# Kernel tuning notes

Hardware: AMD Instinct MI355X
Metric: run time of the kernel (lower is better)

The kernel has to match this reference:

```python
import jax, jax.numpy as jnp
import numpy as np

MD = 4                  # corr_md
D = 2 * MD + 1          # patch_size = 9


def setup_inputs() -> dict:
    key = jax.random.key(0)
    k1, k2 = jax.random.split(key)
    b, c, h, w = 4, 128, 128, 256
    t1 = jax.random.normal(k1, (b, c, h, w), dtype=jnp.float32)
    t2 = jax.random.normal(k2, (b, c, h, w), dtype=jnp.float32)
    return {"t1": t1, "t2": t2}


def reference(t1, t2):
    # Local cost volume: for each displacement (di, dj) in [-MD, MD]^2,
    # out[b, p, y, x] = sum_c t1[b, c, y, x] * t2[b, c, y+di, x+dj]
    # with zero padding outside t2 (SpatialCorrelationSampler semantics,
    # kernel_size=1, stride=1, dilation_patch=1; no channel normalization).
    b, c, h, w = t1.shape
    t2p = jnp.pad(t2, ((0, 0), (0, 0), (MD, MD), (MD, MD)))
    # Loop over the fixed 9x9 displacement grid (81 small reductions);
    outs = [
        jnp.einsum('bchw,bchw->bhw', t1, t2p[:, :, i:i + h, j:j + w])
        for i in range(D) for j in range(D)
    ]
    return jnp.stack(outs, axis=1)  # [b, 81, h, w]
```

## Files before the change

### kernel.cpp

```cpp
#include <hip/hip_runtime.h>

#define NP 81
#define CC 128
#define HH 128
#define WW 256
#define YPAD 136
#define XPAD 272
#define WS_NEED (4ull * YPAD * XPAD * CC * 2ull)

#define SX 16
#define NBLK 1024

typedef __attribute__((ext_vector_type(4))) short bf16x4;
typedef __attribute__((ext_vector_type(8))) short short8;
typedef __attribute__((ext_vector_type(4))) float f32x4;
typedef __attribute__((ext_vector_type(16))) float f32x16;

__device__ __forceinline__ short f2bf(float f) {
    unsigned int u = __builtin_bit_cast(unsigned int, f);
    u += 0x7fffu + ((u >> 16) & 1u);
    return (short)(u >> 16);
}

__global__ __launch_bounds__(256) void prepass_t2t(const float* __restrict__ t2,
                                                   short* __restrict__ ws) {
    const int blk = blockIdx.x;
    const int hf  = blk & 1;
    const int row = blk >> 1;
    const int yp  = row % YPAD;
    const int b   = row / YPAD;
    const int tid = threadIdx.x;
    short* wrow = ws + (size_t)row * XPAD * CC;
    const int y2 = yp - 4;
    const short8 z = {0,0,0,0,0,0,0,0};
    if (y2 < 0 || y2 >= HH) {
        for (int u = tid + hf * 2176; u < 2176 + hf * 2176; u += 256)
            *(short8*)&wrow[(size_t)u * 8] = z;
        return;
    }
    if (tid < 128) {
        const int idx = hf * 8 + (tid >> 4);
        const int xp  = (idx < 4) ? idx : idx + 256;
        *(short8*)&wrow[(size_t)xp * CC + (tid & 15) * 8] = z;
    }
    const size_t plane = (size_t)HH * WW;
#pragma unroll
    for (int i = 0; i < 2; ++i) {
        const int u   = tid + i * 256;
        const int oct = hf * 8 + (u & 7);
        const int xq  = u >> 3;
        const float* p = t2 + ((size_t)(b * CC + oct * 8) * HH + y2) * WW + xq * 4;
        f32x4 v[8];
#pragma unroll
        for (int j = 0; j < 8; ++j) v[j] = *(const f32x4*)&p[(size_t)j * plane];
#pragma unroll
        for (int jj = 0; jj < 4; ++jj) {
            short8 s;
#pragma unroll
            for (int j = 0; j < 8; ++j) s[j] = f2bf(v[j][jj]);
            *(short8*)&wrow[(size_t)(4 + xq * 4 + jj) * CC + oct * 8] = s;
        }
    }
}

__global__ __launch_bounds__(1024) void corr_main16(
        const float* __restrict__ t1, const short* __restrict__ ws,
        float* __restrict__ out) {
    const int bid = blockIdx.x;
    const int sw  = (bid & 7) * (NBLK / 8) + (bid >> 3);
    const int xt = sw & 15;
    const int ys = (sw >> 4) & 15;
    const int b  = sw >> 8;
    const int X0 = xt * SX;
    const int y0 = ys * 8;

    const int tid  = threadIdx.x;
    const int lane = tid & 63;
    const int w    = tid >> 6;
    const int n    = lane & 31;
    const int g    = lane >> 5;

    __shared__ short sA[8 * SX * 128];
    __shared__ __align__(16) float obufs[16 * 9 * 20];

    const short* bp = ws + ((size_t)(b * YPAD + y0 + w) * XPAD + X0 + n) * CC
                    + g * 8;
    short8 bre[8];
#pragma unroll
    for (int kc = 0; kc < 8; ++kc)
        bre[kc] = *(const short8*)&bp[kc * 16];

    if (tid < 512) {
        const int oct = tid & 15;
        const int xq  = (tid >> 4) & 3;
        const int yy  = tid >> 6;
        const size_t plane = (size_t)HH * WW;
        const float* p = t1 + ((size_t)(b * CC + oct * 8) * HH + y0 + yy) * WW
                       + X0 + xq * 4;
#pragma unroll
        for (int h = 0; h < 2; ++h) {
            f32x4 v[4];
#pragma unroll
            for (int j = 0; j < 4; ++j)
                v[j] = *(const f32x4*)&p[(size_t)(h * 4 + j) * plane];
#pragma unroll
            for (int jj = 0; jj < 4; ++jj) {
                const int x = xq * 4 + jj;
                bf16x4 s;
#pragma unroll
                for (int j = 0; j < 4; ++j) s[j] = f2bf(v[j][jj]);
                *(bf16x4*)&sA[yy * 2048 + x * 128 + ((oct ^ x) * 8) + h * 4] = s;
            }
        }
    }
    __syncthreads();

    const int ylo = (w > 8) ? (w - 8) : 0;
    const int yhi = (w < 7) ? w : 7;
    float* ob = &obufs[w * 180];

    for (int yy = ylo; yy <= yhi; ++yy) {
        const int sbase = yy * 2048 + n * 128;

        f32x16 a;
#pragma unroll
        for (int q = 0; q < 16; ++q) a[q] = 0.f;
#pragma unroll
        for (int kc = 0; kc < 8; ++kc) {
            const short8 af = *(const short8*)
                &sA[sbase + (((kc * 2 + g) ^ (n & 15)) * 8)];
            a = __builtin_amdgcn_mfma_f32_32x32x16_bf16(af, bre[kc], a, 0, 0, 0);
        }

#pragma unroll
        for (int q = 0; q < 16; ++q) {
            const int m  = (q & 3) + 8 * (q >> 2) + 4 * g;
            const int dj = n - m;
            if (dj >= 0 && dj <= 8 && m < SX) ob[dj * 20 + m] = a[q];
        }

        const int di = w - yy;
        const int y  = y0 + yy;
        if (lane < 36) {
            const int dj = lane >> 2, xq = lane & 3;
            f32x4 vv = *(const f32x4*)&ob[dj * 20 + xq * 4];
            *(f32x4*)&out[((size_t)(b * NP + di * 9 + dj) * HH + y) * WW
                          + X0 + xq * 4] = vv;
        }
    }
}

#define FB_SX 24
#define FB_NXT 11
#define FB_NBLK (FB_NXT * 16 * 4)
__global__ __launch_bounds__(1024) void corr_fallback(
        const float* __restrict__ t1, const float* __restrict__ t2,
        float* __restrict__ out) {
    const int bid = blockIdx.x;
    const int sw  = (bid & 7) * (FB_NBLK / 8) + (bid >> 3);
    const int ys = sw & 15;
    const int v  = sw >> 4;
    const int xt = v % FB_NXT;
    const int b  = v / FB_NXT;
    const int X0 = xt * FB_SX;
    const int y0 = ys * 8;
    const int tid  = threadIdx.x;
    const int lane = tid & 63;
    const int w    = tid >> 6;
    const int n    = lane & 31;
    const int g    = lane >> 5;
    __shared__ short sA[8 * FB_SX * 128];
    __shared__ __align__(16) float obufs[16 * 9 * 28];
    const size_t plane = (size_t)HH * WW;
    const int r = y0 - 4 + w;
#pragma unroll
    for (int i = 0; i < 3; ++i) {
        const int unit = tid + i * 1024;
        const int x    = unit % FB_SX;
        const int rest = unit / FB_SX;
        const int oct  = rest & 15;
        const int yy   = rest >> 4;
        short8 pk = {0,0,0,0,0,0,0,0};
        if (X0 + x < WW) {
            const float* p = t1 + ((size_t)(b * CC + oct * 8) * HH + (y0 + yy)) * WW
                           + X0 + x;
#pragma unroll
            for (int j = 0; j < 8; ++j) pk[j] = f2bf(p[(size_t)j * plane]);
        }
        *(short8*)&sA[yy * (FB_SX * 128) + x * 128 + ((oct ^ (x & 15)) * 8)] = pk;
    }
    __syncthreads();
    const int x2 = X0 - 4 + n;
    const bool ok = (r >= 0) && (r < HH) && (x2 >= 0) && (x2 < WW);
    const int rc  = r  < 0 ? 0 : (r  > HH - 1 ? HH - 1 : r);
    const int xc  = x2 < 0 ? 0 : (x2 > WW - 1 ? WW - 1 : x2);
    const float* bp = t2 + ((size_t)(b * CC + g * 8) * HH + rc) * WW + xc;
    short8 bre[8];
#pragma unroll
    for (int kc = 0; kc < 8; ++kc) {
        short8 f;
#pragma unroll
        for (int j = 0; j < 8; ++j) f[j] = f2bf(bp[(size_t)(kc * 16 + j) * plane]);
        if (!ok) f = (short8){0,0,0,0,0,0,0,0};
        bre[kc] = f;
    }
    const int ylo = (w > 8) ? (w - 8) : 0;
    const int yhi = (w < 7) ? w : 7;
    float* ob = &obufs[w * 252];
    for (int yy = ylo; yy <= yhi; ++yy) {
        const int sbase = yy * (FB_SX * 128) + n * 128;
        f32x16 a;
#pragma unroll
        for (int q = 0; q < 16; ++q) a[q] = 0.f;
#pragma unroll
        for (int kc = 0; kc < 8; ++kc) {
            const short8 af = *(const short8*)
                &sA[sbase + (((kc * 2 + g) ^ (n & 15)) * 8)];
            a = __builtin_amdgcn_mfma_f32_32x32x16_bf16(af, bre[kc], a, 0, 0, 0);
        }
#pragma unroll
        for (int q = 0; q < 16; ++q) {
            const int m  = (q & 3) + 8 * (q >> 2) + 4 * g;
            const int dj = n - m;
            if (dj >= 0 && dj <= 8 && m < FB_SX) ob[dj * 28 + m] = a[q];
        }
        const int di = w - yy;
        const int y  = y0 + yy;
        if (lane < 54) {
            const int dj = lane / 6, xq = lane % 6;
            if (X0 + xq * 4 < WW) {
                f32x4 vv = *(const f32x4*)&ob[dj * 28 + xq * 4];
                *(f32x4*)&out[((size_t)(b * NP + di * 9 + dj) * HH + y) * WW
                              + X0 + xq * 4] = vv;
            }
        }
    }
}

extern "C" void kernel_launch(void* const* d_in, const int* in_sizes, int n_in,
                              void* d_out, int out_size, void* d_ws, size_t ws_size,
                              hipStream_t stream) {
    const float* t1 = (const float*)d_in[0];
    const float* t2 = (const float*)d_in[1];
    if (ws_size >= WS_NEED) {
        short* ws = (short*)d_ws;
        prepass_t2t<<<4 * YPAD * 2, 256, 0, stream>>>(t2, ws);
        corr_main16<<<NBLK, 1024, 0, stream>>>(t1, ws, (float*)d_out);
    } else {
        corr_fallback<<<FB_NBLK, 1024, 0, stream>>>(t1, t2, (float*)d_out);
    }
}
```

Measured before the change: 194.8 us.

## Process two 8-row y tiles per block with wave-balanced B-row reuse

Result: faster. 190.7 us (-2.1%).

```diff
diff --git a/kernel.cpp b/kernel.cpp
--- a/kernel.cpp
+++ b/kernel.cpp
@@ -9,7 +9,7 @@
 #define WS_NEED (4ull * YPAD * XPAD * CC * 2ull)
 
 #define SX 16
-#define NBLK 1024
+#define NBLK 512
 
 typedef __attribute__((ext_vector_type(4))) short bf16x4;
 typedef __attribute__((ext_vector_type(8))) short short8;
@@ -63,16 +63,16 @@
     }
 }
 
-__global__ __launch_bounds__(1024) void corr_main16(
+__global__ __launch_bounds__(1024) void corr_bal(
         const float* __restrict__ t1, const short* __restrict__ ws,
         float* __restrict__ out) {
     const int bid = blockIdx.x;
     const int sw  = (bid & 7) * (NBLK / 8) + (bid >> 3);
-    const int xt = sw & 15;
-    const int ys = (sw >> 4) & 15;
-    const int b  = sw >> 8;
+    const int xt  = sw & 15;
+    const int yp8 = (sw >> 4) & 7;
+    const int b   = sw >> 7;
     const int X0 = xt * SX;
-    const int y0 = ys * 8;
+    const int y0 = yp8 * 16;
 
     const int tid  = threadIdx.x;
     const int lane = tid & 63;
@@ -80,23 +80,25 @@
     const int n    = lane & 31;
     const int g    = lane >> 5;
 
-    __shared__ short sA[8 * SX * 128];
+    __shared__ short sA[2][8 * SX * 128];
     __shared__ __align__(16) float obufs[16 * 9 * 20];
 
-    const short* bp = ws + ((size_t)(b * YPAD + y0 + w) * XPAD + X0 + n) * CC
-                    + g * 8;
+    const short* bp0 = ws + ((size_t)(b * YPAD + y0 + w) * XPAD + X0 + n) * CC
+                     + g * 8;
     short8 bre[8];
 #pragma unroll
-    for (int kc = 0; kc < 8; ++kc)
-        bre[kc] = *(const short8*)&bp[kc * 16];
-
-    if (tid < 512) {
-        const int oct = tid & 15;
-        const int xq  = (tid >> 4) & 3;
-        const int yy  = tid >> 6;
+    for (int kc = 0; kc < 8; ++kc) bre[kc] = *(const short8*)&bp0[kc * 16];
+
+    {
+        const int sid  = tid & 511;
+        const int half = tid >> 9;
+        const int oct = sid & 15;
+        const int xq  = (sid >> 4) & 3;
+        const int yy  = sid >> 6;
         const size_t plane = (size_t)HH * WW;
-        const float* p = t1 + ((size_t)(b * CC + oct * 8) * HH + y0 + yy) * WW
-                       + X0 + xq * 4;
+        const float* p = t1 + ((size_t)(b * CC + oct * 8) * HH
+                               + y0 + half * 8 + yy) * WW + X0 + xq * 4;
+        short* sAh = sA[half];
 #pragma unroll
         for (int h = 0; h < 2; ++h) {
             f32x4 v[4];
@@ -109,45 +111,56 @@
                 bf16x4 s;
 #pragma unroll
                 for (int j = 0; j < 4; ++j) s[j] = f2bf(v[j][jj]);
-                *(bf16x4*)&sA[yy * 2048 + x * 128 + ((oct ^ x) * 8) + h * 4] = s;
+                *(bf16x4*)&sAh[yy * 2048 + x * 128 + ((oct ^ x) * 8) + h * 4] = s;
             }
         }
     }
     __syncthreads();
 
-    const int ylo = (w > 8) ? (w - 8) : 0;
-    const int yhi = (w < 7) ? w : 7;
     float* ob = &obufs[w * 180];
 
-    for (int yy = ylo; yy <= yhi; ++yy) {
-        const int sbase = yy * 2048 + n * 128;
-
-        f32x16 a;
-#pragma unroll
-        for (int q = 0; q < 16; ++q) a[q] = 0.f;
-#pragma unroll
-        for (int kc = 0; kc < 8; ++kc) {
-            const short8 af = *(const short8*)
-                &sA[sbase + (((kc * 2 + g) ^ (n & 15)) * 8)];
-            a = __builtin_amdgcn_mfma_f32_32x32x16_bf16(af, bre[kc], a, 0, 0, 0);
-        }
-
-#pragma unroll
-        for (int q = 0; q < 16; ++q) {
-            const int m  = (q & 3) + 8 * (q >> 2) + 4 * g;
-            const int dj = n - m;
-            if (dj >= 0 && dj <= 8 && m < SX) ob[dj * 20 + m] = a[q];
-        }
-
-        const int di = w - yy;
-        const int y  = y0 + yy;
-        if (lane < 36) {
-            const int dj = lane >> 2, xq = lane & 3;
-            f32x4 vv = *(const f32x4*)&ob[dj * 20 + xq * 4];
-            *(f32x4*)&out[((size_t)(b * NP + di * 9 + dj) * HH + y) * WW
-                          + X0 + xq * 4] = vv;
-        }
-    }
+    auto run = [&](const short* sAs, int p, int ybase) {
+        const int ylo = (p > 8) ? (p - 8) : 0;
+        const int yhi = (p < 7) ? p : 7;
+        for (int yy = ylo; yy <= yhi; ++yy) {
+            const int sbase = yy * 2048 + n * 128;
+            f32x16 a;
+#pragma unroll
+            for (int q = 0; q < 16; ++q) a[q] = 0.f;
+#pragma unroll
+            for (int kc = 0; kc < 8; ++kc) {
+                const short8 af = *(const short8*)
+                    &sAs[sbase + (((kc * 2 + g) ^ (n & 15)) * 8)];
+                a = __builtin_amdgcn_mfma_f32_32x32x16_bf16(af, bre[kc], a, 0, 0, 0);
+            }
+#pragma unroll
+            for (int q = 0; q < 16; ++q) {
+                const int m  = (q & 3) + 8 * (q >> 2) + 4 * g;
+                const int dj = n - m;
+                if (dj >= 0 && dj <= 8 && m < SX) ob[dj * 20 + m] = a[q];
+            }
+            const int di = p - yy;
+            const int y  = ybase + yy;
+            if (lane < 36) {
+                const int dj = lane >> 2, xq = lane & 3;
+                f32x4 vv = *(const f32x4*)&ob[dj * 20 + xq * 4];
+                *(f32x4*)&out[((size_t)(b * NP + di * 9 + dj) * HH + y) * WW
+                              + X0 + xq * 4] = vv;
+            }
+        }
+    };
+
+    run(sA[0], w, y0);
+
+    if (w < 8) {
+        asm volatile("" ::: "memory");
+        const short* bp1 = ws + ((size_t)(b * YPAD + y0 + 16 + w) * XPAD
+                                 + X0 + n) * CC + g * 8;
+#pragma unroll
+        for (int kc = 0; kc < 8; ++kc) bre[kc] = *(const short8*)&bp1[kc * 16];
+    }
+
+    run(sA[1], (w + 8) & 15, y0 + 8);
 }
 
 #define FB_SX 24
@@ -169,8 +182,8 @@
     const int w    = tid >> 6;
     const int n    = lane & 31;
     const int g    = lane >> 5;
-    __shared__ short sA[8 * FB_SX * 128];
-    __shared__ __align__(16) float obufs[16 * 9 * 28];
+    __shared__ short sAf[8 * FB_SX * 128];
+    __shared__ __align__(16) float obufsf[16 * 9 * 28];
     const size_t plane = (size_t)HH * WW;
     const int r = y0 - 4 + w;
 #pragma unroll
@@ -187,7 +200,7 @@
 #pragma unroll
             for (int j = 0; j < 8; ++j) pk[j] = f2bf(p[(size_t)j * plane]);
         }
-        *(short8*)&sA[yy * (FB_SX * 128) + x * 128 + ((oct ^ (x & 15)) * 8)] = pk;
+        *(short8*)&sAf[yy * (FB_SX * 128) + x * 128 + ((oct ^ (x & 15)) * 8)] = pk;
     }
     __syncthreads();
     const int x2 = X0 - 4 + n;
@@ -206,7 +219,7 @@
     }
     const int ylo = (w > 8) ? (w - 8) : 0;
     const int yhi = (w < 7) ? w : 7;
-    float* ob = &obufs[w * 252];
+    float* ob = &obufsf[w * 252];
     for (int yy = ylo; yy <= yhi; ++yy) {
         const int sbase = yy * (FB_SX * 128) + n * 128;
         f32x16 a;
@@ -215,7 +228,7 @@
 #pragma unroll
         for (int kc = 0; kc < 8; ++kc) {
             const short8 af = *(const short8*)
-                &sA[sbase + (((kc * 2 + g) ^ (n & 15)) * 8)];
+                &sAf[sbase + (((kc * 2 + g) ^ (n & 15)) * 8)];
             a = __builtin_amdgcn_mfma_f32_32x32x16_bf16(af, bre[kc], a, 0, 0, 0);
         }
 #pragma unroll
@@ -245,7 +258,7 @@
     if (ws_size >= WS_NEED) {
         short* ws = (short*)d_ws;
         prepass_t2t<<<4 * YPAD * 2, 256, 0, stream>>>(t2, ws);
-        corr_main16<<<NBLK, 1024, 0, stream>>>(t1, ws, (float*)d_out);
+        corr_bal<<<NBLK, 1024, 0, stream>>>(t1, ws, (float*)d_out);
     } else {
         corr_fallback<<<FB_NBLK, 1024, 0, stream>>>(t1, t2, (float*)d_out);
     }
```
